# Kernel tuning notes

Hardware: AMD Instinct MI355X
Metric: run time of the kernel (lower is better)

Reference implementation:

```python
import jax, jax.numpy as jnp
import numpy as np

TOP_K = 2
TEMP = 1.0

def setup_inputs() -> dict:
    key = jax.random.key(0)
    ks = jax.random.split(key, 7)
    B, T, D, E = 2, 2048, 768, 8
    F = 4 * D
    s = 0.02
    return {
        "x": jax.random.normal(ks[0], (B, T, D), dtype=jnp.float32),
        "gate_w": jax.random.normal(ks[1], (D, E), dtype=jnp.float32) * s,
        "gate_b": jnp.zeros((E,), dtype=jnp.float32),
        "w1": jax.random.normal(ks[2], (E, D, F), dtype=jnp.float32) * s,
        "b1": jnp.zeros((E, F), dtype=jnp.float32),
        "w2": jax.random.normal(ks[3], (E, F, D), dtype=jnp.float32) * s,
        "b2": jnp.zeros((E, D), dtype=jnp.float32),
    }

def reference(x, gate_w, gate_b, w1, b1, w2, b2):
    B, T, D = x.shape
    E = gate_w.shape[1]
    x_flat = x.reshape(-1, D)                       # [N, D]
    logits = x_flat @ gate_w + gate_b              # [N, E]
    gates = jax.nn.softmax(logits / TEMP, axis=-1)
    topk_gates, topk_idx = jax.lax.top_k(gates, TOP_K)   # [N, K]
    topk_gates = topk_gates / (jnp.sum(topk_gates, axis=-1, keepdims=True) + 1e-9)
    # Dense combine weights: w[n, e] = sum_k topk_gates[n, k] * (topk_idx[n, k] == e)
    combine = jnp.sum(
        topk_gates[:, :, None] * jax.nn.one_hot(topk_idx, E, dtype=x.dtype),
        axis=1,
    )                                               # [N, E]
    out = jnp.zeros_like(x_flat)
    for e in range(E):  # fixed small expert loop (structurally distinct params)
        h = jax.nn.gelu(x_flat @ w1[e] + b1[e], approximate=False)  # [N, 4D]
        y = h @ w2[e] + b2[e]                                       # [N, D]
        out = out + combine[:, e:e + 1] * y
    return out.reshape(B, T, D)
```

## Files before the change

### kernel.cpp

```cpp
#include <hip/hip_runtime.h>
#include <hip/hip_bf16.h>


#define N_TOK 4096
#define DIM   768
#define FDIM  3072
#define NEXP  8

typedef __attribute__((ext_vector_type(8))) _Float16 f16x8;
typedef __attribute__((ext_vector_type(4))) _Float16 f16x4;
typedef __attribute__((ext_vector_type(4))) float     f32x4;

__device__ __forceinline__ float gelu_exact(float v) {
    return 0.5f * v * (1.0f + erff(v * 0.7071067811865475f));
}

__device__ __forceinline__ void gload_lds16(const _Float16* g, _Float16* l) {
    __builtin_amdgcn_global_load_lds(
        (const __attribute__((address_space(1))) void*)g,
        (__attribute__((address_space(3))) void*)l,
        16, 0, 0);
}

__global__ __launch_bounds__(256) void cast_x_kernel(const float* __restrict__ x,
                                                     _Float16* __restrict__ xh) {
    int i = blockIdx.x * 256 + threadIdx.x;
    float4 v = ((const float4*)x)[i];
    f16x4 o;
    o[0] = (_Float16)v.x; o[1] = (_Float16)v.y;
    o[2] = (_Float16)v.z; o[3] = (_Float16)v.w;
    ((f16x4*)xh)[i] = o;
}

__global__ __launch_bounds__(256) void transpose_cast_kernel(const float* __restrict__ in,
                                                             _Float16* __restrict__ out,
                                                             int R, int C) {
    const int e  = blockIdx.z;
    const size_t eoff = (size_t)e * R * C;
    const int c0 = blockIdx.x * 64;
    const int r0 = blockIdx.y * 64;
    __shared__ _Float16 tile[64][66];
    const int t = threadIdx.x;
    #pragma unroll
    for (int it = 0; it < 4; it++) {
        int lin = it * 256 + t;
        int r  = lin >> 4;
        int c4 = lin & 15;
        float4 v = *(const float4*)&in[eoff + (size_t)(r0 + r) * C + c0 + c4 * 4];
        tile[r][c4 * 4 + 0] = (_Float16)v.x;
        tile[r][c4 * 4 + 1] = (_Float16)v.y;
        tile[r][c4 * 4 + 2] = (_Float16)v.z;
        tile[r][c4 * 4 + 3] = (_Float16)v.w;
    }
    __syncthreads();
    #pragma unroll
    for (int it = 0; it < 4; it++) {
        int lin = it * 256 + t;
        int c  = lin >> 4;
        int r4 = lin & 15;
        f16x4 o;
        #pragma unroll
        for (int j = 0; j < 4; j++) o[j] = tile[r4 * 4 + j][c];
        *(f16x4*)&out[eoff + (size_t)(c0 + c) * R + r0 + r4 * 4] = o;
    }
}

__global__ __launch_bounds__(256) void gate_kernel(const float* __restrict__ x,
                                                   const float* __restrict__ gw,
                                                   const float* __restrict__ gb,
                                                   int* __restrict__ tok_list,
                                                   float* __restrict__ wt_list,
                                                   int* __restrict__ count) {
    const int gtid = blockIdx.x * 256 + threadIdx.x;
    const int n    = gtid >> 6;
    const int lane = threadIdx.x & 63;
    if (n >= N_TOK) return;
    double part[NEXP];
    #pragma unroll
    for (int e = 0; e < NEXP; e++) part[e] = 0.0;
    for (int d = lane; d < DIM; d += 64) {
        float xv = x[n * DIM + d];
        const float* g = &gw[d * NEXP];
        #pragma unroll
        for (int e = 0; e < NEXP; e++) part[e] += (double)xv * (double)g[e];
    }
    #pragma unroll
    for (int e = 0; e < NEXP; e++) {
        double v = part[e];
        #pragma unroll
        for (int off = 32; off > 0; off >>= 1) v += __shfl_xor(v, off);
        part[e] = v + (double)gb[e];
    }
    if (lane == 0) {
        double mx = part[0];
        #pragma unroll
        for (int e = 1; e < NEXP; e++) mx = fmax(mx, part[e]);
        double ex[NEXP]; double s = 0.0;
        #pragma unroll
        for (int e = 0; e < NEXP; e++) { ex[e] = exp(part[e] - mx); s += ex[e]; }
        int i0 = 0;
        #pragma unroll
        for (int e = 1; e < NEXP; e++) if (ex[e] > ex[i0]) i0 = e;
        int i1 = (i0 == 0) ? 1 : 0;
        #pragma unroll
        for (int e = 0; e < NEXP; e++) if (e != i0 && ex[e] > ex[i1]) i1 = e;
        float g0 = (float)(ex[i0] / s), g1 = (float)(ex[i1] / s);
        float dn = g0 + g1 + 1e-9f;
        float w0 = g0 / dn, w1 = g1 / dn;
        int s0 = atomicAdd(&count[i0], 1);
        tok_list[i0 * N_TOK + s0] = n;  wt_list[i0 * N_TOK + s0] = w0;
        int s1 = atomicAdd(&count[i1], 1);
        tok_list[i1 * N_TOK + s1] = n;  wt_list[i1 * N_TOK + s1] = w1;
    }
}

__global__ void scan_kernel(const int* __restrict__ count, int* __restrict__ basep) {
    if (threadIdx.x == 0) {
        int s = 0;
        for (int e = 0; e < NEXP; e++) { basep[e] = s; s += count[e]; }
    }
}

__global__ __launch_bounds__(256) void mm1_kernel(const _Float16* __restrict__ xh,
                                                  const _Float16* __restrict__ w1t,
                                                  const float* __restrict__ bias1,
                                                  const int* __restrict__ tok_list,
                                                  const int* __restrict__ count,
                                                  const int* __restrict__ basep,
                                                  _Float16* __restrict__ h) {
    const int e    = blockIdx.y;
    const int cnt  = count[e];
    const int row0 = blockIdx.z * 128;
    if (row0 >= cnt) return;
    const int col0 = blockIdx.x * 128;
    const int t    = threadIdx.x;
    const int lane = t & 63;
    const int wv   = t >> 6;
    const int wy   = wv >> 1, wx = wv & 1;
    const int m_lane = lane & 15, quad = lane >> 4;

    __shared__ __align__(16) _Float16 As[3][128][32];
    __shared__ __align__(16) _Float16 Bs[3][128][32];

    const int srow = t >> 2;
    const int kin  = (t & 3) * 8;

    int i0 = row0 + srow;      if (i0 > cnt - 1) i0 = cnt - 1;
    int i1 = row0 + 64 + srow; if (i1 > cnt - 1) i1 = cnt - 1;
    const int tokA0 = tok_list[e * N_TOK + i0];
    const int tokA1 = tok_list[e * N_TOK + i1];
    const _Float16* pa0 = xh + (size_t)tokA0 * DIM + kin;
    const _Float16* pa1 = xh + (size_t)tokA1 * DIM + kin;
    const _Float16* pb0 = w1t + (size_t)e * FDIM * DIM + (size_t)(col0 + srow) * DIM + kin;
    const _Float16* pb1 = pb0 + (size_t)64 * DIM;

    f32x4 acc[4][4];
    #pragma unroll
    for (int i = 0; i < 4; i++)
        #pragma unroll
        for (int j = 0; j < 4; j++)
            acc[i][j] = (f32x4){0.f, 0.f, 0.f, 0.f};

    const int NT = DIM / 32;

    asm volatile("s_waitcnt vmcnt(0)" ::: "memory");
    gload_lds16(pa0, &As[0][srow][kin]);
    gload_lds16(pa1, &As[0][64 + srow][kin]);
    gload_lds16(pb0, &Bs[0][srow][kin]);
    gload_lds16(pb1, &Bs[0][64 + srow][kin]);
    gload_lds16(pa0 + 32, &As[1][srow][kin]);
    gload_lds16(pa1 + 32, &As[1][64 + srow][kin]);
    gload_lds16(pb0 + 32, &Bs[1][srow][kin]);
    gload_lds16(pb1 + 32, &Bs[1][64 + srow][kin]);

    int cur = 0;
    for (int ti = 0; ti < NT; ++ti) {
        if (ti == NT - 1) asm volatile("s_waitcnt vmcnt(0) lgkmcnt(0)" ::: "memory");
        else              asm volatile("s_waitcnt vmcnt(4) lgkmcnt(0)" ::: "memory");
        __builtin_amdgcn_s_barrier();
        asm volatile("" ::: "memory");
        if (ti + 2 < NT) {
            int nb = cur + 2; if (nb >= 3) nb -= 3;
            int kk = (ti + 2) * 32;
            gload_lds16(pa0 + kk, &As[nb][srow][kin]);
            gload_lds16(pa1 + kk, &As[nb][64 + srow][kin]);
            gload_lds16(pb0 + kk, &Bs[nb][srow][kin]);
            gload_lds16(pb1 + kk, &Bs[nb][64 + srow][kin]);
        }
        f16x8 af[4], bf[4];
        #pragma unroll
        for (int i = 0; i < 4; i++)
            af[i] = *(const f16x8*)&As[cur][wy * 64 + i * 16 + m_lane][quad * 8];
        #pragma unroll
        for (int j = 0; j < 4; j++)
            bf[j] = *(const f16x8*)&Bs[cur][wx * 64 + j * 16 + m_lane][quad * 8];
        #pragma unroll
        for (int i = 0; i < 4; i++)
            #pragma unroll
            for (int j = 0; j < 4; j++)
                acc[i][j] = __builtin_amdgcn_mfma_f32_16x16x32_f16(af[i], bf[j], acc[i][j], 0, 0, 0);
        cur = cur + 1; if (cur >= 3) cur = 0;
    }

    const int hbase = basep[e];
    #pragma unroll
    for (int i = 0; i < 4; i++) {
        #pragma unroll
        for (int r = 0; r < 4; r++) {
            int rl = wy * 64 + i * 16 + quad * 4 + r;
            int gr = row0 + rl;
            if (gr < cnt) {
                _Float16* hrow = h + (size_t)(hbase + gr) * FDIM;
                #pragma unroll
                for (int j = 0; j < 4; j++) {
                    int c = col0 + wx * 64 + j * 16 + m_lane;
                    float v = acc[i][j][r] + bias1[e * FDIM + c];
                    hrow[c] = (_Float16)gelu_exact(v);
                }
            }
        }
    }
}

__global__ __launch_bounds__(256) void mm2_kernel(const _Float16* __restrict__ h,
                                                  const _Float16* __restrict__ w2t,
                                                  const float* __restrict__ bias2,
                                                  const int* __restrict__ tok_list,
                                                  const float* __restrict__ wt_list,
                                                  const int* __restrict__ count,
                                                  const int* __restrict__ basep,
                                                  float* __restrict__ out) {
    const int e    = blockIdx.y >> 1;
    const int ks   = blockIdx.y & 1;
    const int cnt  = count[e];
    const int row0 = blockIdx.z * 128;
    if (row0 >= cnt) return;
    const int col0 = blockIdx.x * 128;
    const int t    = threadIdx.x;
    const int lane = t & 63;
    const int wv   = t >> 6;
    const int wy   = wv >> 1, wx = wv & 1;
    const int m_lane = lane & 15, quad = lane >> 4;

    __shared__ __align__(16) _Float16 As[3][128][32];
    __shared__ __align__(16) _Float16 Bs[3][128][32];

    const int srow = t >> 2;
    const int kin  = (t & 3) * 8;

    const int hbase = basep[e];
    int i0 = row0 + srow;      if (i0 > cnt - 1) i0 = cnt - 1;
    int i1 = row0 + 64 + srow; if (i1 > cnt - 1) i1 = cnt - 1;
    const size_t koff = (size_t)ks * (FDIM / 2);
    const _Float16* pa0 = h + (size_t)(hbase + i0) * FDIM + koff + kin;
    const _Float16* pa1 = h + (size_t)(hbase + i1) * FDIM + koff + kin;
    const _Float16* pb0 = w2t + (size_t)e * DIM * FDIM + (size_t)(col0 + srow) * FDIM + koff + kin;
    const _Float16* pb1 = pb0 + (size_t)64 * FDIM;

    f32x4 acc[4][4];
    #pragma unroll
    for (int i = 0; i < 4; i++)
        #pragma unroll
        for (int j = 0; j < 4; j++)
            acc[i][j] = (f32x4){0.f, 0.f, 0.f, 0.f};

    const int NT = (FDIM / 2) / 32;

    asm volatile("s_waitcnt vmcnt(0)" ::: "memory");
    gload_lds16(pa0, &As[0][srow][kin]);
    gload_lds16(pa1, &As[0][64 + srow][kin]);
    gload_lds16(pb0, &Bs[0][srow][kin]);
    gload_lds16(pb1, &Bs[0][64 + srow][kin]);
    gload_lds16(pa0 + 32, &As[1][srow][kin]);
    gload_lds16(pa1 + 32, &As[1][64 + srow][kin]);
    gload_lds16(pb0 + 32, &Bs[1][srow][kin]);
    gload_lds16(pb1 + 32, &Bs[1][64 + srow][kin]);

    int cur = 0;
    for (int ti = 0; ti < NT; ++ti) {
        if (ti == NT - 1) asm volatile("s_waitcnt vmcnt(0) lgkmcnt(0)" ::: "memory");
        else              asm volatile("s_waitcnt vmcnt(4) lgkmcnt(0)" ::: "memory");
        __builtin_amdgcn_s_barrier();
        asm volatile("" ::: "memory");
        if (ti + 2 < NT) {
            int nb = cur + 2; if (nb >= 3) nb -= 3;
            int kk = (ti + 2) * 32;
            gload_lds16(pa0 + kk, &As[nb][srow][kin]);
            gload_lds16(pa1 + kk, &As[nb][64 + srow][kin]);
            gload_lds16(pb0 + kk, &Bs[nb][srow][kin]);
            gload_lds16(pb1 + kk, &Bs[nb][64 + srow][kin]);
        }
        f16x8 af[4], bf[4];
        #pragma unroll
        for (int i = 0; i < 4; i++)
            af[i] = *(const f16x8*)&As[cur][wy * 64 + i * 16 + m_lane][quad * 8];
        #pragma unroll
        for (int j = 0; j < 4; j++)
            bf[j] = *(const f16x8*)&Bs[cur][wx * 64 + j * 16 + m_lane][quad * 8];
        #pragma unroll
        for (int i = 0; i < 4; i++)
            #pragma unroll
            for (int j = 0; j < 4; j++)
                acc[i][j] = __builtin_amdgcn_mfma_f32_16x16x32_f16(af[i], bf[j], acc[i][j], 0, 0, 0);
        cur = cur + 1; if (cur >= 3) cur = 0;
    }

    #pragma unroll
    for (int i = 0; i < 4; i++) {
        #pragma unroll
        for (int r = 0; r < 4; r++) {
            int rl = wy * 64 + i * 16 + quad * 4 + r;
            int gr = row0 + rl;
            if (gr < cnt) {
                int tok   = tok_list[e * N_TOK + gr];
                float wgt = wt_list[e * N_TOK + gr];
                float* orow = out + (size_t)tok * DIM;
                #pragma unroll
                for (int j = 0; j < 4; j++) {
                    int c = col0 + wx * 64 + j * 16 + m_lane;
                    float v = acc[i][j][r] + ((ks == 0) ? bias2[e * DIM + c] : 0.f);
                    atomicAdd(&orow[c], wgt * v);
                }
            }
        }
    }
}

extern "C" void kernel_launch(void* const* d_in, const int* in_sizes, int n_in,
                              void* d_out, int out_size, void* d_ws, size_t ws_size,
                              hipStream_t stream) {
    const float* x  = (const float*)d_in[0];
    const float* gw = (const float*)d_in[1];
    const float* gb = (const float*)d_in[2];
    const float* w1 = (const float*)d_in[3];
    const float* b1 = (const float*)d_in[4];
    const float* w2 = (const float*)d_in[5];
    const float* b2 = (const float*)d_in[6];
    float* out = (float*)d_out;

    char* ws = (char*)d_ws;
    _Float16* xh   = (_Float16*)ws;
    _Float16* w1t  = xh  + (size_t)N_TOK * DIM;
    _Float16* w2t  = w1t + (size_t)NEXP * FDIM * DIM;
    _Float16* hbuf = w2t + (size_t)NEXP * DIM * FDIM;
    int*   tok_list = (int*)(hbuf + (size_t)2 * N_TOK * FDIM);
    float* wt_list  = (float*)(tok_list + NEXP * N_TOK);
    int*   count    = (int*)(wt_list + NEXP * N_TOK);
    int*   basep    = count + 8;

    hipMemsetAsync(count, 0, 64, stream);
    hipMemsetAsync(out, 0, (size_t)out_size * sizeof(float), stream);

    cast_x_kernel<<<dim3(N_TOK * DIM / 4 / 256), 256, 0, stream>>>(x, xh);
    transpose_cast_kernel<<<dim3(FDIM / 64, DIM / 64, NEXP), 256, 0, stream>>>(w1, w1t, DIM, FDIM);
    transpose_cast_kernel<<<dim3(DIM / 64, FDIM / 64, NEXP), 256, 0, stream>>>(w2, w2t, FDIM, DIM);
    gate_kernel<<<dim3(N_TOK / 4), 256, 0, stream>>>(x, gw, gb, tok_list, wt_list, count);
    scan_kernel<<<1, 64, 0, stream>>>(count, basep);
    mm1_kernel<<<dim3(FDIM / 128, NEXP, N_TOK / 128), 256, 0, stream>>>(
        xh, w1t, b1, tok_list, count, basep, hbuf);
    mm2_kernel<<<dim3(DIM / 128, NEXP * 2, N_TOK / 128), 256, 0, stream>>>(
        hbuf, w2t, b2, tok_list, wt_list, count, basep, out);
}
```

Baseline: 556.7 us.

## Switch GEMMs to double-buffered LDS pipeline and merge weight transpose launches

Both expert GEMM kernels drop the three-stage LDS ring with explicit vmcnt waits and raw barriers, and use a simpler two-buffer scheme with __syncthreads after each k-step. This cuts LDS use per block, which may allow more resident blocks, but prefetch runs only one tile ahead and each step pays a full barrier and drain. The two weight transpose-cast launches are also merged into one kernel that picks w1 or w2 from the grid y index, saving a launch. Correctness of the double buffer relies on __syncthreads waiting for the async global-to-LDS loads to finish.

```diff
diff --git a/kernel.cpp b/kernel.cpp
--- a/kernel.cpp
+++ b/kernel.cpp
@@ -32,13 +32,19 @@
     ((f16x4*)xh)[i] = o;
 }
 
-__global__ __launch_bounds__(256) void transpose_cast_kernel(const float* __restrict__ in,
-                                                             _Float16* __restrict__ out,
-                                                             int R, int C) {
-    const int e  = blockIdx.z;
+__global__ __launch_bounds__(256) void transpose_cast2_kernel(const float* __restrict__ w1,
+                                                              const float* __restrict__ w2,
+                                                              _Float16* __restrict__ w1t,
+                                                              _Float16* __restrict__ w2t) {
+    const int z     = blockIdx.y;
+    const int which = z >> 3;
+    const int e     = z & 7;
+    const float* in; _Float16* out; int R, C, tx, ty;
+    if (which == 0) { in = w1; out = w1t; R = DIM;  C = FDIM; tx = blockIdx.x % (FDIM / 64); ty = blockIdx.x / (FDIM / 64); }
+    else            { in = w2; out = w2t; R = FDIM; C = DIM;  tx = blockIdx.x % (DIM  / 64); ty = blockIdx.x / (DIM  / 64); }
     const size_t eoff = (size_t)e * R * C;
-    const int c0 = blockIdx.x * 64;
-    const int r0 = blockIdx.y * 64;
+    const int c0 = tx * 64;
+    const int r0 = ty * 64;
     __shared__ _Float16 tile[64][66];
     const int t = threadIdx.x;
     #pragma unroll
@@ -139,8 +145,8 @@
     const int wy   = wv >> 1, wx = wv & 1;
     const int m_lane = lane & 15, quad = lane >> 4;
 
-    __shared__ __align__(16) _Float16 As[3][128][32];
-    __shared__ __align__(16) _Float16 Bs[3][128][32];
+    __shared__ __align__(16) _Float16 As[2][128][32];
+    __shared__ __align__(16) _Float16 Bs[2][128][32];
 
     const int srow = t >> 2;
     const int kin  = (t & 3) * 8;
@@ -163,25 +169,17 @@
 
     const int NT = DIM / 32;
 
-    asm volatile("s_waitcnt vmcnt(0)" ::: "memory");
     gload_lds16(pa0, &As[0][srow][kin]);
     gload_lds16(pa1, &As[0][64 + srow][kin]);
     gload_lds16(pb0, &Bs[0][srow][kin]);
     gload_lds16(pb1, &Bs[0][64 + srow][kin]);
-    gload_lds16(pa0 + 32, &As[1][srow][kin]);
-    gload_lds16(pa1 + 32, &As[1][64 + srow][kin]);
-    gload_lds16(pb0 + 32, &Bs[1][srow][kin]);
-    gload_lds16(pb1 + 32, &Bs[1][64 + srow][kin]);
+    __syncthreads();
 
     int cur = 0;
     for (int ti = 0; ti < NT; ++ti) {
-        if (ti == NT - 1) asm volatile("s_waitcnt vmcnt(0) lgkmcnt(0)" ::: "memory");
-        else              asm volatile("s_waitcnt vmcnt(4) lgkmcnt(0)" ::: "memory");
-        __builtin_amdgcn_s_barrier();
-        asm volatile("" ::: "memory");
-        if (ti + 2 < NT) {
-            int nb = cur + 2; if (nb >= 3) nb -= 3;
-            int kk = (ti + 2) * 32;
+        if (ti + 1 < NT) {
+            int kk = (ti + 1) * 32;
+            int nb = cur ^ 1;
             gload_lds16(pa0 + kk, &As[nb][srow][kin]);
             gload_lds16(pa1 + kk, &As[nb][64 + srow][kin]);
             gload_lds16(pb0 + kk, &Bs[nb][srow][kin]);
@@ -199,7 +197,8 @@
             #pragma unroll
             for (int j = 0; j < 4; j++)
                 acc[i][j] = __builtin_amdgcn_mfma_f32_16x16x32_f16(af[i], bf[j], acc[i][j], 0, 0, 0);
-        cur = cur + 1; if (cur >= 3) cur = 0;
+        __syncthreads();
+        cur ^= 1;
     }
 
     const int hbase = basep[e];
@@ -242,8 +241,8 @@
     const int wy   = wv >> 1, wx = wv & 1;
     const int m_lane = lane & 15, quad = lane >> 4;
 
-    __shared__ __align__(16) _Float16 As[3][128][32];
-    __shared__ __align__(16) _Float16 Bs[3][128][32];
+    __shared__ __align__(16) _Float16 As[2][128][32];
+    __shared__ __align__(16) _Float16 Bs[2][128][32];
 
     const int srow = t >> 2;
     const int kin  = (t & 3) * 8;
@@ -266,25 +265,17 @@
 
     const int NT = (FDIM / 2) / 32;
 
-    asm volatile("s_waitcnt vmcnt(0)" ::: "memory");
     gload_lds16(pa0, &As[0][srow][kin]);
     gload_lds16(pa1, &As[0][64 + srow][kin]);
     gload_lds16(pb0, &Bs[0][srow][kin]);
     gload_lds16(pb1, &Bs[0][64 + srow][kin]);
-    gload_lds16(pa0 + 32, &As[1][srow][kin]);
-    gload_lds16(pa1 + 32, &As[1][64 + srow][kin]);
-    gload_lds16(pb0 + 32, &Bs[1][srow][kin]);
-    gload_lds16(pb1 + 32, &Bs[1][64 + srow][kin]);
+    __syncthreads();
 
     int cur = 0;
     for (int ti = 0; ti < NT; ++ti) {
-        if (ti == NT - 1) asm volatile("s_waitcnt vmcnt(0) lgkmcnt(0)" ::: "memory");
-        else              asm volatile("s_waitcnt vmcnt(4) lgkmcnt(0)" ::: "memory");
-        __builtin_amdgcn_s_barrier();
-        asm volatile("" ::: "memory");
-        if (ti + 2 < NT) {
-            int nb = cur + 2; if (nb >= 3) nb -= 3;
-            int kk = (ti + 2) * 32;
+        if (ti + 1 < NT) {
+            int kk = (ti + 1) * 32;
+            int nb = cur ^ 1;
             gload_lds16(pa0 + kk, &As[nb][srow][kin]);
             gload_lds16(pa1 + kk, &As[nb][64 + srow][kin]);
             gload_lds16(pb0 + kk, &Bs[nb][srow][kin]);
@@ -302,7 +293,8 @@
             #pragma unroll
             for (int j = 0; j < 4; j++)
                 acc[i][j] = __builtin_amdgcn_mfma_f32_16x16x32_f16(af[i], bf[j], acc[i][j], 0, 0, 0);
-        cur = cur + 1; if (cur >= 3) cur = 0;
+        __syncthreads();
+        cur ^= 1;
     }
 
     #pragma unroll
@@ -352,8 +344,7 @@
     hipMemsetAsync(out, 0, (size_t)out_size * sizeof(float), stream);
 
     cast_x_kernel<<<dim3(N_TOK * DIM / 4 / 256), 256, 0, stream>>>(x, xh);
-    transpose_cast_kernel<<<dim3(FDIM / 64, DIM / 64, NEXP), 256, 0, stream>>>(w1, w1t, DIM, FDIM);
-    transpose_cast_kernel<<<dim3(DIM / 64, FDIM / 64, NEXP), 256, 0, stream>>>(w2, w2t, FDIM, DIM);
+    transpose_cast2_kernel<<<dim3(576, 16), 256, 0, stream>>>(w1, w2, w1t, w2t);
     gate_kernel<<<dim3(N_TOK / 4), 256, 0, stream>>>(x, gw, gb, tok_list, wt_list, count);
     scan_kernel<<<1, 64, 0, stream>>>(count, basep);
     mm1_kernel<<<dim3(FDIM / 128, NEXP, N_TOK / 128), 256, 0, stream>>>(
```

After: 531.8 us. 4.5% less time.
